# Performance work log

Measured on AMD Instinct MI355X. Metric: run time of the kernel, lower is better.

The kernel has to match this reference:

```python
import jax, jax.numpy as jnp
import numpy as np

B, Q, K = 4, 2048, 2048
D_IN = 1024
H, D_ATN, D_V, D_OUT = 16, 64, 64, 1024
NEG = -1e10


def setup_inputs() -> dict:
    key = jax.random.key(0)
    ks = jax.random.split(key, 8)
    queries = jax.random.normal(ks[0], (B, Q, D_IN), dtype=jnp.float32)
    keys = jax.random.normal(ks[1], (B, K, D_IN), dtype=jnp.float32)
    values = jax.random.normal(ks[2], (B, K, D_IN), dtype=jnp.float32)
    mask = jax.random.randint(ks[3], (B, Q, K), 0, 2, dtype=jnp.int32)
    s = 1.0 / np.sqrt(D_IN)
    Wq = jax.random.normal(ks[4], (D_IN, D_ATN * H), dtype=jnp.float32) * s
    Wk = jax.random.normal(ks[5], (D_IN, D_ATN * H), dtype=jnp.float32) * s
    Wv = jax.random.normal(ks[6], (D_IN, D_V * H), dtype=jnp.float32) * s
    Wo = jax.random.normal(ks[7], (H * D_V, D_OUT), dtype=jnp.float32) * (1.0 / np.sqrt(H * D_V))
    return {"queries": queries, "keys": keys, "values": values, "mask": mask,
            "Wq": Wq, "Wk": Wk, "Wv": Wv, "Wo": Wo}


def reference(queries, keys, values, mask, Wq, Wk, Wv, Wo):
    # project and split heads as in torch: view(B, S, -1, num_heads) -> head axis LAST
    qs = (queries @ Wq).reshape(B, Q, D_ATN, H)  # [b, i, d, h]
    ks = (keys @ Wk).reshape(B, K, D_ATN, H)     # [b, o, d, h]
    vs = (values @ Wv).reshape(B, K, D_V, H)     # [b, o, d, h]
    scale = jnp.sqrt(jnp.asarray(D_ATN, dtype=qs.dtype))
    w = jnp.einsum('bidh,bodh->bioh', qs, ks) / scale  # [b, i, o, h]
    w = jnp.where(mask[..., None] == 0, NEG, w)
    w = jax.nn.softmax(w, axis=-2)  # softmax over keys (o) axis
    mha = jnp.einsum('bioh,bodh->bidh', w, vs).reshape(B, Q, D_V * H)
    return mha @ Wo
```

## Files before the change

### kernel.cpp

```cpp
#include <hip/hip_runtime.h>


typedef __bf16 bf16x8 __attribute__((ext_vector_type(8)));
typedef __bf16 bf16x4 __attribute__((ext_vector_type(4)));
typedef float f32x4 __attribute__((ext_vector_type(4)));

__device__ __forceinline__ unsigned short f2bf(float f) {
  union { float f; unsigned u; } x; x.f = f;
  unsigned r = x.u + 0x7fffu + ((x.u >> 16) & 1u);
  return (unsigned short)(r >> 16);
}

__device__ __forceinline__ f32x4 mfma16(bf16x8 a, bf16x8 b, f32x4 c) {
  return __builtin_amdgcn_mfma_f32_16x16x32_bf16(a, b, c, 0, 0, 0);
}

__device__ __forceinline__ void gl16(const void* g, void* l) {
  __builtin_amdgcn_global_load_lds(
      (const __attribute__((address_space(1))) unsigned int*)g,
      (__attribute__((address_space(3))) unsigned int*)l, 16, 0, 0);
}

__device__ __forceinline__ int permf(int x) { return ((x & 15) << 6) | (x >> 4); }
__device__ __forceinline__ int ipermf(int x) { return ((x & 63) << 4) | (x >> 6); }

__global__ __launch_bounds__(256) void wtrans_k(const float* __restrict__ W0,
                                                const float* __restrict__ W1,
                                                const float* __restrict__ W2,
                                                const float* __restrict__ W3,
                                                unsigned short* __restrict__ T0,
                                                unsigned short* __restrict__ T1,
                                                unsigned short* __restrict__ T2,
                                                unsigned short* __restrict__ T3) {
  const int z = blockIdx.z;
  const float* W = z == 0 ? W0 : z == 1 ? W1 : z == 2 ? W2 : W3;
  unsigned short* T = z == 0 ? T0 : z == 1 ? T1 : z == 2 ? T2 : T3;
  __shared__ float t[32][33];
  int n0 = blockIdx.x * 32, k0 = blockIdx.y * 32;
  int tx = threadIdx.x, ty = threadIdx.y;
#pragma unroll
  for (int r = 0; r < 32; r += 8) {
    int srow = (z == 3) ? ipermf(k0 + ty + r) : (k0 + ty + r);
    t[ty + r][tx] = W[(long)srow * 1024 + n0 + tx];
  }
  __syncthreads();
#pragma unroll
  for (int r = 0; r < 32; r += 8) {
    int drow = (z < 3) ? permf(n0 + ty + r) : (n0 + ty + r);
    T[(long)drow * 1024 + k0 + tx] = f2bf(t[tx][ty + r]);
  }
}

__global__ __launch_bounds__(256) void maskbits_k(const int* __restrict__ m,
                                                  unsigned long long* __restrict__ mb) {
  long i = (long)blockIdx.x * 256 + threadIdx.x;
  unsigned long long b = __ballot(m[i] != 0);
  if ((threadIdx.x & 63) == 0) mb[i >> 6] = b;
}

__global__ __launch_bounds__(256) void cvt_k(const float* __restrict__ q,
                                             const float* __restrict__ k,
                                             const float* __restrict__ v,
                                             unsigned short* __restrict__ o0,
                                             unsigned short* __restrict__ o1,
                                             unsigned short* __restrict__ o2) {
  const float* in = blockIdx.y == 0 ? q : blockIdx.y == 1 ? k : v;
  unsigned short* out = blockIdx.y == 0 ? o0 : blockIdx.y == 1 ? o1 : o2;
  long i = ((long)blockIdx.x * 256 + threadIdx.x) * 8;
  float4 a = *(const float4*)(in + i);
  float4 b = *(const float4*)(in + i + 4);
  union { bf16x8 v8; uint4 u; } o;
  o.v8[0] = (__bf16)a.x; o.v8[1] = (__bf16)a.y; o.v8[2] = (__bf16)a.z; o.v8[3] = (__bf16)a.w;
  o.v8[4] = (__bf16)b.x; o.v8[5] = (__bf16)b.y; o.v8[6] = (__bf16)b.z; o.v8[7] = (__bf16)b.w;
  *(uint4*)(out + i) = o.u;
}

template <int OUTMODE>
__global__ __launch_bounds__(256, 2) void gemm2_k(const unsigned short* __restrict__ A,
                                                  const unsigned short* __restrict__ Bt,
                                                  void* __restrict__ Out, float scale) {
  __shared__ __align__(16) char lds[2][32768];
  const int t = threadIdx.x, lane = t & 63, wv = t >> 6;
  const int wm = wv >> 1, wn = wv & 1;
  const int id = blockIdx.x;
  const int logical = (id & 7) * 64 + (id >> 3);
  const int i0 = (logical >> 3) * 128, n0 = (logical & 7) * 128;
  const int lr = lane & 15, lg = lane >> 4;

  long aoff[4], boff[4];
#pragma unroll
  for (int j = 0; j < 4; ++j) {
    int c = j * 256 + t, r = c >> 3, kc = (c & 7) ^ (r & 7);
    aoff[j] = ((long)(i0 + r) << 10) + kc * 8;
    boff[j] = ((long)(n0 + r) << 10) + kc * 8;
  }

  f32x4 zero = {0.f, 0.f, 0.f, 0.f};
  f32x4 acc[4][4];
#pragma unroll
  for (int mt = 0; mt < 4; ++mt)
#pragma unroll
    for (int nt = 0; nt < 4; ++nt) acc[mt][nt] = zero;

#pragma unroll
  for (int j = 0; j < 4; ++j) {
    gl16(A + aoff[j], &lds[0][j * 4096 + wv * 1024]);
    gl16(Bt + boff[j], &lds[0][16384 + j * 4096 + wv * 1024]);
  }
  __syncthreads();

  for (int ks = 0; ks < 16; ++ks) {
    const int cur = ks & 1;
    if (ks + 1 < 16) {
      const unsigned short* Ak = A + (ks + 1) * 64;
      const unsigned short* Bk = Bt + (ks + 1) * 64;
#pragma unroll
      for (int j = 0; j < 4; ++j) {
        gl16(Ak + aoff[j], &lds[cur ^ 1][j * 4096 + wv * 1024]);
        gl16(Bk + boff[j], &lds[cur ^ 1][16384 + j * 4096 + wv * 1024]);
      }
    }
    const char* Ab = &lds[cur][0];
    const char* Bb = &lds[cur][16384];
    bf16x8 af[2][4], bfr[2][4];
#pragma unroll
    for (int mt = 0; mt < 4; ++mt) {
      int r = wm * 64 + mt * 16 + lr;
      int sw = (r & 7) << 4;
      af[0][mt] = *(const bf16x8*)(Ab + r * 128 + ((lg * 16) ^ sw));
      af[1][mt] = *(const bf16x8*)(Ab + r * 128 + ((64 + lg * 16) ^ sw));
    }
#pragma unroll
    for (int nt = 0; nt < 4; ++nt) {
      int r = wn * 64 + nt * 16 + lr;
      int sw = (r & 7) << 4;
      bfr[0][nt] = *(const bf16x8*)(Bb + r * 128 + ((lg * 16) ^ sw));
      bfr[1][nt] = *(const bf16x8*)(Bb + r * 128 + ((64 + lg * 16) ^ sw));
    }
#pragma unroll
    for (int h2 = 0; h2 < 2; ++h2)
#pragma unroll
      for (int mt = 0; mt < 4; ++mt)
#pragma unroll
        for (int nt = 0; nt < 4; ++nt)
          acc[mt][nt] = mfma16(af[h2][mt], bfr[h2][nt], acc[mt][nt]);
    __syncthreads();
  }

  if (OUTMODE == 2) {
    float* O = (float*)Out;
#pragma unroll
    for (int mt = 0; mt < 4; ++mt)
#pragma unroll
      for (int nt = 0; nt < 4; ++nt)
#pragma unroll
        for (int r = 0; r < 4; ++r) {
          int row = i0 + wm * 64 + mt * 16 + lg * 4 + r;
          int col = n0 + wn * 64 + nt * 16 + lr;
          O[(long)row * 1024 + col] = acc[mt][nt][r];
        }
  } else if (OUTMODE == 0) {
    unsigned short* O = (unsigned short*)Out;
#pragma unroll
    for (int mt = 0; mt < 4; ++mt)
#pragma unroll
      for (int nt = 0; nt < 4; ++nt) {
        int col = n0 + wn * 64 + nt * 16 + lr;
        int h = col >> 6, d = col & 63;
#pragma unroll
        for (int r = 0; r < 4; ++r) {
          int row = i0 + wm * 64 + mt * 16 + lg * 4 + r;
          int b = row >> 11, s = row & 2047;
          O[(((long)(b * 16 + h) * 2048 + s) << 6) + d] = f2bf(acc[mt][nt][r] * scale);
        }
      }
  } else if (OUTMODE == 3) {
    char* O = (char*)Out;
#pragma unroll
    for (int mt = 0; mt < 4; ++mt)
#pragma unroll
      for (int nt = 0; nt < 4; ++nt) {
        int col = n0 + wn * 64 + nt * 16 + lr;
        int h = col >> 6, d = col & 63;
#pragma unroll
        for (int r = 0; r < 4; ++r) {
          int row = i0 + wm * 64 + mt * 16 + lg * 4 + r;
          int b = row >> 11, s = row & 2047;
          int bh = b * 16 + h, ts = s >> 6, key = s & 63;
          long byte = ((long)(bh * 32 + ts) << 13) + key * 128 + ((d * 2) ^ ((key & 7) << 4));
          unsigned short bv = f2bf(acc[mt][nt][r]);
          *(unsigned short*)(O + byte) = bv;
        }
      }
  } else {
    char* O = (char*)Out;
#pragma unroll
    for (int mt = 0; mt < 4; ++mt)
#pragma unroll
      for (int nt = 0; nt < 4; ++nt) {
        int col = n0 + wn * 64 + nt * 16 + lr;
        int h = col >> 6, d = col & 63;
        int row0 = i0 + wm * 64 + mt * 16 + lg * 4;
        int b = row0 >> 11, s0 = row0 & 2047;
        int bh = b * 16 + h, ts = s0 >> 6, key0 = s0 & 63;
        ushort4 w;
        w.x = f2bf(acc[mt][nt][0]); w.y = f2bf(acc[mt][nt][1]);
        w.z = f2bf(acc[mt][nt][2]); w.w = f2bf(acc[mt][nt][3]);
        long byte = ((long)(bh * 32 + ts) << 13) + d * 128 + ((key0 * 2) ^ ((d & 7) << 4));
        *(ushort4*)(O + byte) = w;
      }
  }
}

__global__ __launch_bounds__(256, 3) void attn_k(const unsigned short* __restrict__ Qh,
                                                 const unsigned short* __restrict__ Kh,
                                                 const unsigned short* __restrict__ Vt,
                                                 const unsigned long long* __restrict__ MB,
                                                 unsigned short* __restrict__ Mha) {
  __shared__ __align__(16) char kv[2][16384];
  __shared__ __align__(16) char P[4][4096];
  __shared__ __align__(16) float LUT[64];
  const int t = threadIdx.x, lane = t & 63, wv = t >> 6;
  const int id = blockIdx.x;
  const int logical = (id & 7) * 128 + (id >> 3);
  const int bh = logical >> 4, qt = logical & 15;
  const int b = bh >> 4, h = bh & 15;
  const int i0 = qt * 128 + wv * 32;
  const int lr = lane & 15, lg = lane >> 4;

  const unsigned short* Qp = Qh + ((long)bh * 2048 + i0) * 64;
  const char* Kg = (const char*)Kh + ((long)bh << 18);
  const char* Vg = (const char*)Vt + ((long)bh << 18);
  const unsigned long long* mrow0 = MB + ((long)b * 2048 + i0 + lr) * 32;
  const unsigned long long* mrow1 = mrow0 + 16 * 32;
  char* Pw = &P[wv][0];
  const char* LUTb = (const char*)LUT;
  const int swz = (lr & 7) << 4;
  const int goff = wv * 2048 + lane * 16;
  const int loff = wv * 2048;

  if (t < 16) {
    f32x4 e;
    e[0] = (t & 1) ? 0.f : -30000.f;
    e[1] = (t & 2) ? 0.f : -30000.f;
    e[2] = (t & 4) ? 0.f : -30000.f;
    e[3] = (t & 8) ? 0.f : -30000.f;
    *(f32x4*)&LUT[t * 4] = e;
  }

  bf16x8 qf00 = *(const bf16x8*)(Qp + lr * 64 + lg * 8);
  bf16x8 qf01 = *(const bf16x8*)(Qp + lr * 64 + 32 + lg * 8);
  bf16x8 qf10 = *(const bf16x8*)(Qp + (16 + lr) * 64 + lg * 8);
  bf16x8 qf11 = *(const bf16x8*)(Qp + (16 + lr) * 64 + 32 + lg * 8);

  bf16x8 ones;
#pragma unroll
  for (int i = 0; i < 8; ++i) ones[i] = (__bf16)1.0f;

  f32x4 zero = {0.f, 0.f, 0.f, 0.f};
  f32x4 oa0[4], oa1[4];
#pragma unroll
  for (int dt = 0; dt < 4; ++dt) { oa0[dt] = zero; oa1[dt] = zero; }
  float l0 = 0.f, l1 = 0.f;

  {
    char* dst = &kv[0][0];
    gl16(Kg + goff, dst + loff);
    gl16(Kg + goff + 1024, dst + loff + 1024);
    gl16(Vg + goff, dst + 8192 + loff);
    gl16(Vg + goff + 1024, dst + 8192 + loff + 1024);
  }
  __syncthreads();

  for (int ts = 0; ts < 32; ++ts) {
    const int cur = ts & 1;
    if (ts + 1 < 32) {
      const char* kg = Kg + ((long)(ts + 1) << 13);
      const char* vg = Vg + ((long)(ts + 1) << 13);
      char* dst = &kv[cur ^ 1][0];
      gl16(kg + goff, dst + loff);
      gl16(kg + goff + 1024, dst + loff + 1024);
      gl16(vg + goff, dst + 8192 + loff);
      gl16(vg + goff + 1024, dst + 8192 + loff + 1024);
    }
    unsigned long long m64_0 = mrow0[ts] >> (4 * lg);
    unsigned long long m64_1 = mrow1[ts] >> (4 * lg);
    unsigned lo0 = (unsigned)m64_0, hi0 = (unsigned)(m64_0 >> 32);
    unsigned lo1 = (unsigned)m64_1, hi1 = (unsigned)(m64_1 >> 32);
    f32x4 z0[4], z1[4];
    z0[0] = *(const f32x4*)(LUTb + ((lo0 << 4) & 0xF0));
    z0[1] = *(const f32x4*)(LUTb + ((lo0 >> 12) & 0xF0));
    z0[2] = *(const f32x4*)(LUTb + ((hi0 << 4) & 0xF0));
    z0[3] = *(const f32x4*)(LUTb + ((hi0 >> 12) & 0xF0));
    z1[0] = *(const f32x4*)(LUTb + ((lo1 << 4) & 0xF0));
    z1[1] = *(const f32x4*)(LUTb + ((lo1 >> 12) & 0xF0));
    z1[2] = *(const f32x4*)(LUTb + ((hi1 << 4) & 0xF0));
    z1[3] = *(const f32x4*)(LUTb + ((hi1 >> 12) & 0xF0));

    const char* Kb = &kv[cur][0];
    const char* Vb = &kv[cur][8192];
    f32x4 sv0[4], sv1[4];
#pragma unroll
    for (int nt = 0; nt < 4; ++nt) {
      int key = nt * 16 + lr;
      int ksz = (key & 7) << 4;
      bf16x8 kf0 = *(const bf16x8*)(Kb + key * 128 + ((lg * 16) ^ ksz));
      bf16x8 kf1 = *(const bf16x8*)(Kb + key * 128 + ((lg * 16 + 64) ^ ksz));
      sv0[nt] = mfma16(kf1, qf01, mfma16(kf0, qf00, z0[nt]));
      sv1[nt] = mfma16(kf1, qf11, mfma16(kf0, qf10, z1[nt]));
    }
#pragma unroll
    for (int nt = 0; nt < 4; ++nt)
#pragma unroll
      for (int r = 0; r < 4; ++r) {
        sv0[nt][r] = exp2f(sv0[nt][r]);
        sv1[nt][r] = exp2f(sv1[nt][r]);
      }
#pragma unroll
    for (int nt = 0; nt < 4; ++nt) {
      bf16x4 w0, w1;
      w0[0] = (__bf16)sv0[nt][0]; w0[1] = (__bf16)sv0[nt][1];
      w0[2] = (__bf16)sv0[nt][2]; w0[3] = (__bf16)sv0[nt][3];
      w1[0] = (__bf16)sv1[nt][0]; w1[1] = (__bf16)sv1[nt][1];
      w1[2] = (__bf16)sv1[nt][2]; w1[3] = (__bf16)sv1[nt][3];
      *(bf16x4*)(Pw + lr * 128 + ((32 * nt + 8 * lg) ^ swz)) = w0;
      *(bf16x4*)(Pw + 2048 + lr * 128 + ((32 * nt + 8 * lg) ^ swz)) = w1;
    }
    bf16x8 pa00 = *(const bf16x8*)(Pw + lr * 128 + ((16 * lg) ^ swz));
    bf16x8 pa01 = *(const bf16x8*)(Pw + lr * 128 + ((64 + 16 * lg) ^ swz));
    bf16x8 pa10 = *(const bf16x8*)(Pw + 2048 + lr * 128 + ((16 * lg) ^ swz));
    bf16x8 pa11 = *(const bf16x8*)(Pw + 2048 + lr * 128 + ((64 + 16 * lg) ^ swz));
    f32x4 rsv0 = mfma16(ones, pa01, mfma16(ones, pa00, zero));
    f32x4 rsv1 = mfma16(ones, pa11, mfma16(ones, pa10, zero));
    l0 += rsv0[0];
    l1 += rsv1[0];
#pragma unroll
    for (int dt = 0; dt < 4; ++dt) {
      int d = dt * 16 + lr;
      int vsz = (d & 7) << 4;
      bf16x8 vf0 = *(const bf16x8*)(Vb + d * 128 + ((lg * 16) ^ vsz));
      bf16x8 vf1 = *(const bf16x8*)(Vb + d * 128 + ((lg * 16 + 64) ^ vsz));
      oa0[dt] = mfma16(vf0, pa00, oa0[dt]);
      oa0[dt] = mfma16(vf1, pa01, oa0[dt]);
      oa1[dt] = mfma16(vf0, pa10, oa1[dt]);
      oa1[dt] = mfma16(vf1, pa11, oa1[dt]);
    }
    __syncthreads();
  }
  float inv0 = 1.f / l0, inv1 = 1.f / l1;
#pragma unroll
  for (int dt = 0; dt < 4; ++dt) {
    bf16x4 w0, w1;
#pragma unroll
    for (int r = 0; r < 4; ++r) { w0[r] = (__bf16)(oa0[dt][r] * inv0); w1[r] = (__bf16)(oa1[dt][r] * inv1); }
    int byte = lr * 128 + ((dt * 32 + lg * 8) ^ swz);
    *(bf16x4*)(Pw + byte) = w0;
    *(bf16x4*)(Pw + 2048 + byte) = w1;
  }
  unsigned short* Op = Mha + ((long)b * 2048 + i0 + lr) * 1024 + h * 64 + lg * 16;
  {
    int b0 = lr * 128 + ((lg * 32) ^ swz);
    int b1 = lr * 128 + ((lg * 32 + 16) ^ swz);
    uint4 lo0 = *(const uint4*)(Pw + b0), hi0 = *(const uint4*)(Pw + b1);
    uint4 lo1 = *(const uint4*)(Pw + 2048 + b0), hi1 = *(const uint4*)(Pw + 2048 + b1);
    *(uint4*)(Op) = lo0;            *(uint4*)(Op + 8) = hi0;
    *(uint4*)(Op + 16 * 1024) = lo1; *(uint4*)(Op + 16 * 1024 + 8) = hi1;
  }
}

extern "C" void kernel_launch(void* const* d_in, const int* in_sizes, int n_in,
                              void* d_out, int out_size, void* d_ws, size_t ws_size,
                              hipStream_t stream) {
  const float* q = (const float*)d_in[0];
  const float* k = (const float*)d_in[1];
  const float* v = (const float*)d_in[2];
  const int* mask = (const int*)d_in[3];
  const float* Wq = (const float*)d_in[4];
  const float* Wk = (const float*)d_in[5];
  const float* Wv = (const float*)d_in[6];
  const float* Wo = (const float*)d_in[7];
  (void)in_sizes; (void)n_in; (void)out_size; (void)ws_size;

  char* ws = (char*)d_ws;
  unsigned short* Wqt = (unsigned short*)(ws + (0ul << 20));
  unsigned short* Wkt = (unsigned short*)(ws + (2ul << 20));
  unsigned short* Wvt = (unsigned short*)(ws + (4ul << 20));
  unsigned short* Wot = (unsigned short*)(ws + (6ul << 20));
  unsigned long long* MBp = (unsigned long long*)(ws + (8ul << 20));
  unsigned short* Qh  = (unsigned short*)(ws + (10ul << 20));
  unsigned short* Kh  = (unsigned short*)(ws + (26ul << 20));
  unsigned short* Vt  = (unsigned short*)(ws + (42ul << 20));
  unsigned short* Mha = (unsigned short*)(ws + (58ul << 20));
  unsigned short* X1 = Mha, *X2 = Qh, *X3 = Kh;

  wtrans_k<<<dim3(32, 32, 4), dim3(32, 8), 0, stream>>>(Wq, Wk, Wv, Wo, Wqt, Wkt, Wvt, Wot);
  maskbits_k<<<65536, 256, 0, stream>>>(mask, MBp);
  cvt_k<<<dim3(4096, 3), 256, 0, stream>>>(q, k, v, X1, X2, X3);

  gemm2_k<4><<<512, 256, 0, stream>>>(X3, Wvt, Vt, 1.0f);
  gemm2_k<3><<<512, 256, 0, stream>>>(X2, Wkt, Kh, 1.0f);
  gemm2_k<0><<<512, 256, 0, stream>>>(X1, Wqt, Qh, 0.125f * 1.44269504f);

  attn_k<<<1024, 256, 0, stream>>>(Qh, Kh, Vt, MBp, Mha);

  gemm2_k<2><<<512, 256, 0, stream>>>(Mha, Wot, d_out, 1.0f);
}
```

Baseline: 275.0 us.

## Enlarge attention query tile per wave and keep P in registers via permlane swaps

The attention kernel now gives each wave 64 query rows instead of 32 and each block 256 queries, halving the grid. Every K/V tile loaded into shared memory is therefore reused across twice as many queries. The P matrix no longer round-trips through LDS: it is packed with v_cvt_pk_bf16_f32 and rearranged with permlane32/16 swaps into the MFMA operand layout. The mask bias is built from bit arithmetic instead of an LDS lookup table, and exp2 uses the hardware builtin. The cost is higher register pressure (launch bound occupancy drops from 3 to 2) and fewer blocks to fill the GPU.

```diff
diff --git a/kernel.cpp b/kernel.cpp
--- a/kernel.cpp
+++ b/kernel.cpp
@@ -11,6 +11,14 @@
   return (unsigned short)(r >> 16);
 }
 
+__device__ __forceinline__ float exp2fast(float x) {
+#if __has_builtin(__builtin_amdgcn_exp2f)
+  return __builtin_amdgcn_exp2f(x);
+#else
+  return exp2f(x);
+#endif
+}
+
 __device__ __forceinline__ f32x4 mfma16(bf16x8 a, bf16x8 b, f32x4 c) {
   return __builtin_amdgcn_mfma_f32_16x16x32_bf16(a, b, c, 0, 0, 0);
 }
@@ -19,6 +27,18 @@
   __builtin_amdgcn_global_load_lds(
       (const __attribute__((address_space(1))) unsigned int*)g,
       (__attribute__((address_space(3))) unsigned int*)l, 16, 0, 0);
+}
+
+__device__ __forceinline__ unsigned cvtpk(float lo, float hi) {
+  unsigned r;
+  asm("v_cvt_pk_bf16_f32 %0, %1, %2" : "=v"(r) : "v"(lo), "v"(hi));
+  return r;
+}
+__device__ __forceinline__ void swap32(unsigned &a, unsigned &b) {
+  asm("v_permlane32_swap_b32 %0, %1" : "+v"(a), "+v"(b));
+}
+__device__ __forceinline__ void swap16(unsigned &a, unsigned &b) {
+  asm("v_permlane16_swap_b32 %0, %1" : "+v"(a), "+v"(b));
 }
 
 __device__ __forceinline__ int permf(int x) { return ((x & 15) << 6) | (x >> 4); }
@@ -212,56 +232,48 @@
   }
 }
 
-__global__ __launch_bounds__(256, 3) void attn_k(const unsigned short* __restrict__ Qh,
+__global__ __launch_bounds__(256, 2) void attn_k(const unsigned short* __restrict__ Qh,
                                                  const unsigned short* __restrict__ Kh,
                                                  const unsigned short* __restrict__ Vt,
                                                  const unsigned long long* __restrict__ MB,
                                                  unsigned short* __restrict__ Mha) {
   __shared__ __align__(16) char kv[2][16384];
-  __shared__ __align__(16) char P[4][4096];
-  __shared__ __align__(16) float LUT[64];
   const int t = threadIdx.x, lane = t & 63, wv = t >> 6;
   const int id = blockIdx.x;
-  const int logical = (id & 7) * 128 + (id >> 3);
-  const int bh = logical >> 4, qt = logical & 15;
+  const int logical = (id & 7) * 64 + (id >> 3);
+  const int bh = logical >> 3, qt = logical & 7;
   const int b = bh >> 4, h = bh & 15;
-  const int i0 = qt * 128 + wv * 32;
+  const int i0 = qt * 256 + wv * 64;
   const int lr = lane & 15, lg = lane >> 4;
 
   const unsigned short* Qp = Qh + ((long)bh * 2048 + i0) * 64;
   const char* Kg = (const char*)Kh + ((long)bh << 18);
   const char* Vg = (const char*)Vt + ((long)bh << 18);
-  const unsigned long long* mrow0 = MB + ((long)b * 2048 + i0 + lr) * 32;
-  const unsigned long long* mrow1 = mrow0 + 16 * 32;
-  char* Pw = &P[wv][0];
-  const char* LUTb = (const char*)LUT;
+  const unsigned long long* mrow[4];
+#pragma unroll
+  for (int g = 0; g < 4; ++g) mrow[g] = MB + ((long)b * 2048 + i0 + g * 16 + lr) * 32;
   const int swz = (lr & 7) << 4;
   const int goff = wv * 2048 + lane * 16;
   const int loff = wv * 2048;
 
-  if (t < 16) {
-    f32x4 e;
-    e[0] = (t & 1) ? 0.f : -30000.f;
-    e[1] = (t & 2) ? 0.f : -30000.f;
-    e[2] = (t & 4) ? 0.f : -30000.f;
-    e[3] = (t & 8) ? 0.f : -30000.f;
-    *(f32x4*)&LUT[t * 4] = e;
-  }
-
-  bf16x8 qf00 = *(const bf16x8*)(Qp + lr * 64 + lg * 8);
-  bf16x8 qf01 = *(const bf16x8*)(Qp + lr * 64 + 32 + lg * 8);
-  bf16x8 qf10 = *(const bf16x8*)(Qp + (16 + lr) * 64 + lg * 8);
-  bf16x8 qf11 = *(const bf16x8*)(Qp + (16 + lr) * 64 + 32 + lg * 8);
+  bf16x8 qf0[4], qf1[4];
+#pragma unroll
+  for (int g = 0; g < 4; ++g) {
+    qf0[g] = *(const bf16x8*)(Qp + (g * 16 + lr) * 64 + lg * 8);
+    qf1[g] = *(const bf16x8*)(Qp + (g * 16 + lr) * 64 + 32 + lg * 8);
+  }
 
   bf16x8 ones;
 #pragma unroll
   for (int i = 0; i < 8; ++i) ones[i] = (__bf16)1.0f;
 
   f32x4 zero = {0.f, 0.f, 0.f, 0.f};
-  f32x4 oa0[4], oa1[4];
-#pragma unroll
-  for (int dt = 0; dt < 4; ++dt) { oa0[dt] = zero; oa1[dt] = zero; }
-  float l0 = 0.f, l1 = 0.f;
+  f32x4 oa[4][4];
+#pragma unroll
+  for (int g = 0; g < 4; ++g)
+#pragma unroll
+    for (int dt = 0; dt < 4; ++dt) oa[g][dt] = zero;
+  float l[4] = {0.f, 0.f, 0.f, 0.f};
 
   {
     char* dst = &kv[0][0];
@@ -283,88 +295,93 @@
       gl16(vg + goff, dst + 8192 + loff);
       gl16(vg + goff + 1024, dst + 8192 + loff + 1024);
     }
-    unsigned long long m64_0 = mrow0[ts] >> (4 * lg);
-    unsigned long long m64_1 = mrow1[ts] >> (4 * lg);
-    unsigned lo0 = (unsigned)m64_0, hi0 = (unsigned)(m64_0 >> 32);
-    unsigned lo1 = (unsigned)m64_1, hi1 = (unsigned)(m64_1 >> 32);
-    f32x4 z0[4], z1[4];
-    z0[0] = *(const f32x4*)(LUTb + ((lo0 << 4) & 0xF0));
-    z0[1] = *(const f32x4*)(LUTb + ((lo0 >> 12) & 0xF0));
-    z0[2] = *(const f32x4*)(LUTb + ((hi0 << 4) & 0xF0));
-    z0[3] = *(const f32x4*)(LUTb + ((hi0 >> 12) & 0xF0));
-    z1[0] = *(const f32x4*)(LUTb + ((lo1 << 4) & 0xF0));
-    z1[1] = *(const f32x4*)(LUTb + ((lo1 >> 12) & 0xF0));
-    z1[2] = *(const f32x4*)(LUTb + ((hi1 << 4) & 0xF0));
-    z1[3] = *(const f32x4*)(LUTb + ((hi1 >> 12) & 0xF0));
+    unsigned milo[4], mihi[4];
+#pragma unroll
+    for (int g = 0; g < 4; ++g) {
+      unsigned long long ms = mrow[g][ts] >> (4 * lg);
+      milo[g] = ~(unsigned)ms;
+      mihi[g] = ~(unsigned)(ms >> 32);
+    }
 
     const char* Kb = &kv[cur][0];
     const char* Vb = &kv[cur][8192];
-    f32x4 sv0[4], sv1[4];
+    f32x4 sv[4][4];
 #pragma unroll
     for (int nt = 0; nt < 4; ++nt) {
       int key = nt * 16 + lr;
       int ksz = (key & 7) << 4;
       bf16x8 kf0 = *(const bf16x8*)(Kb + key * 128 + ((lg * 16) ^ ksz));
       bf16x8 kf1 = *(const bf16x8*)(Kb + key * 128 + ((lg * 16 + 64) ^ ksz));
-      sv0[nt] = mfma16(kf1, qf01, mfma16(kf0, qf00, z0[nt]));
-      sv1[nt] = mfma16(kf1, qf11, mfma16(kf0, qf10, z1[nt]));
-    }
-#pragma unroll
-    for (int nt = 0; nt < 4; ++nt)
-#pragma unroll
-      for (int r = 0; r < 4; ++r) {
-        sv0[nt][r] = exp2f(sv0[nt][r]);
-        sv1[nt][r] = exp2f(sv1[nt][r]);
+#pragma unroll
+      for (int g = 0; g < 4; ++g) {
+        unsigned w = (nt < 2) ? milo[g] : mihi[g];
+        f32x4 z;
+#pragma unroll
+        for (int r = 0; r < 4; ++r) {
+          int mb = ((int)(w << (31 - ((nt & 1) * 16 + r)))) >> 31;
+          z[r] = __int_as_float(mb & 0xC6EA6000);
+        }
+        sv[g][nt] = mfma16(kf1, qf1[g], mfma16(kf0, qf0[g], z));
       }
-#pragma unroll
-    for (int nt = 0; nt < 4; ++nt) {
-      bf16x4 w0, w1;
-      w0[0] = (__bf16)sv0[nt][0]; w0[1] = (__bf16)sv0[nt][1];
-      w0[2] = (__bf16)sv0[nt][2]; w0[3] = (__bf16)sv0[nt][3];
-      w1[0] = (__bf16)sv1[nt][0]; w1[1] = (__bf16)sv1[nt][1];
-      w1[2] = (__bf16)sv1[nt][2]; w1[3] = (__bf16)sv1[nt][3];
-      *(bf16x4*)(Pw + lr * 128 + ((32 * nt + 8 * lg) ^ swz)) = w0;
-      *(bf16x4*)(Pw + 2048 + lr * 128 + ((32 * nt + 8 * lg) ^ swz)) = w1;
-    }
-    bf16x8 pa00 = *(const bf16x8*)(Pw + lr * 128 + ((16 * lg) ^ swz));
-    bf16x8 pa01 = *(const bf16x8*)(Pw + lr * 128 + ((64 + 16 * lg) ^ swz));
-    bf16x8 pa10 = *(const bf16x8*)(Pw + 2048 + lr * 128 + ((16 * lg) ^ swz));
-    bf16x8 pa11 = *(const bf16x8*)(Pw + 2048 + lr * 128 + ((64 + 16 * lg) ^ swz));
-    f32x4 rsv0 = mfma16(ones, pa01, mfma16(ones, pa00, zero));
-    f32x4 rsv1 = mfma16(ones, pa11, mfma16(ones, pa10, zero));
-    l0 += rsv0[0];
-    l1 += rsv1[0];
+    }
+#pragma unroll
+    for (int g = 0; g < 4; ++g)
+#pragma unroll
+      for (int nt = 0; nt < 4; ++nt)
+#pragma unroll
+        for (int r = 0; r < 4; ++r) sv[g][nt][r] = exp2fast(sv[g][nt][r]);
+    union pu { unsigned w[4]; bf16x8 v; };
+    pu pa0[4], pa1[4];
+#pragma unroll
+    for (int g = 0; g < 4; ++g) {
+      unsigned u00 = cvtpk(sv[g][0][0], sv[g][0][1]), u01 = cvtpk(sv[g][0][2], sv[g][0][3]);
+      unsigned u10 = cvtpk(sv[g][1][0], sv[g][1][1]), u11 = cvtpk(sv[g][1][2], sv[g][1][3]);
+      unsigned u20 = cvtpk(sv[g][2][0], sv[g][2][1]), u21 = cvtpk(sv[g][2][2], sv[g][2][3]);
+      unsigned u30 = cvtpk(sv[g][3][0], sv[g][3][1]), u31 = cvtpk(sv[g][3][2], sv[g][3][3]);
+      swap32(u00, u10); swap16(u00, u10);
+      swap32(u01, u11); swap16(u01, u11);
+      pa0[g].w[0] = u00; pa0[g].w[1] = u01; pa0[g].w[2] = u10; pa0[g].w[3] = u11;
+      swap32(u20, u30); swap16(u20, u30);
+      swap32(u21, u31); swap16(u21, u31);
+      pa1[g].w[0] = u20; pa1[g].w[1] = u21; pa1[g].w[2] = u30; pa1[g].w[3] = u31;
+    }
+#pragma unroll
+    for (int g = 0; g < 4; ++g) {
+      f32x4 rs = mfma16(ones, pa1[g].v, mfma16(ones, pa0[g].v, zero));
+      l[g] += rs[0];
+    }
 #pragma unroll
     for (int dt = 0; dt < 4; ++dt) {
       int d = dt * 16 + lr;
       int vsz = (d & 7) << 4;
       bf16x8 vf0 = *(const bf16x8*)(Vb + d * 128 + ((lg * 16) ^ vsz));
       bf16x8 vf1 = *(const bf16x8*)(Vb + d * 128 + ((lg * 16 + 64) ^ vsz));
-      oa0[dt] = mfma16(vf0, pa00, oa0[dt]);
-      oa0[dt] = mfma16(vf1, pa01, oa0[dt]);
-      oa1[dt] = mfma16(vf0, pa10, oa1[dt]);
-      oa1[dt] = mfma16(vf1, pa11, oa1[dt]);
+#pragma unroll
+      for (int g = 0; g < 4; ++g)
+        oa[g][dt] = mfma16(vf1, pa1[g].v, mfma16(vf0, pa0[g].v, oa[g][dt]));
     }
     __syncthreads();
   }
-  float inv0 = 1.f / l0, inv1 = 1.f / l1;
-#pragma unroll
-  for (int dt = 0; dt < 4; ++dt) {
-    bf16x4 w0, w1;
-#pragma unroll
-    for (int r = 0; r < 4; ++r) { w0[r] = (__bf16)(oa0[dt][r] * inv0); w1[r] = (__bf16)(oa1[dt][r] * inv1); }
-    int byte = lr * 128 + ((dt * 32 + lg * 8) ^ swz);
-    *(bf16x4*)(Pw + byte) = w0;
-    *(bf16x4*)(Pw + 2048 + byte) = w1;
-  }
-  unsigned short* Op = Mha + ((long)b * 2048 + i0 + lr) * 1024 + h * 64 + lg * 16;
-  {
-    int b0 = lr * 128 + ((lg * 32) ^ swz);
-    int b1 = lr * 128 + ((lg * 32 + 16) ^ swz);
-    uint4 lo0 = *(const uint4*)(Pw + b0), hi0 = *(const uint4*)(Pw + b1);
-    uint4 lo1 = *(const uint4*)(Pw + 2048 + b0), hi1 = *(const uint4*)(Pw + 2048 + b1);
-    *(uint4*)(Op) = lo0;            *(uint4*)(Op + 8) = hi0;
-    *(uint4*)(Op + 16 * 1024) = lo1; *(uint4*)(Op + 16 * 1024 + 8) = hi1;
+  char* scr = &kv[0][0] + wv * 8192;
+#pragma unroll
+  for (int g = 0; g < 4; ++g) {
+    float inv = 1.f / l[g];
+#pragma unroll
+    for (int dt = 0; dt < 4; ++dt) {
+      bf16x4 w;
+#pragma unroll
+      for (int r = 0; r < 4; ++r) w[r] = (__bf16)(oa[g][dt][r] * inv);
+      *(bf16x4*)(scr + g * 2048 + lr * 128 + ((dt * 32 + lg * 8) ^ swz)) = w;
+    }
+  }
+#pragma unroll
+  for (int g = 0; g < 4; ++g) {
+    unsigned short* Op = Mha + ((long)b * 2048 + i0 + g * 16 + lr) * 1024 + h * 64 + lg * 16;
+    int b0 = g * 2048 + lr * 128 + ((lg * 32) ^ swz);
+    int b1 = g * 2048 + lr * 128 + ((lg * 32 + 16) ^ swz);
+    uint4 lo = *(const uint4*)(scr + b0), hi = *(const uint4*)(scr + b1);
+    *(uint4*)(Op) = lo;
+    *(uint4*)(Op + 8) = hi;
   }
 }
 
@@ -401,7 +418,7 @@
   gemm2_k<3><<<512, 256, 0, stream>>>(X2, Wkt, Kh, 1.0f);
   gemm2_k<0><<<512, 256, 0, stream>>>(X1, Wqt, Qh, 0.125f * 1.44269504f);
 
-  attn_k<<<1024, 256, 0, stream>>>(Qh, Kh, Vt, MBp, Mha);
+  attn_k<<<512, 256, 0, stream>>>(Qh, Kh, Vt, MBp, Mha);
 
   gemm2_k<2><<<512, 256, 0, stream>>>(Mha, Wot, d_out, 1.0f);
 }
```

New measurement: 252.4 us. -8.2%, faster.
